# Kernel tuning notes

Hardware: AMD Instinct MI355X
Metric: run time of the kernel (lower is better)

## Reference

```python
import jax, jax.numpy as jnp
import numpy as np

NUM_TRACKS = [128, 256, 512, 1024, 2048, 64, 32, 1024]
B, S, D = 8, 2048, 1536
H = len(NUM_TRACKS)
T = max(NUM_TRACKS)  # num_output_tracks (padded)


def setup_inputs() -> dict:
    key = jax.random.key(0)
    kx, kw, kb, ki = jax.random.split(key, 4)
    x = jax.random.normal(kx, (B, S, D), dtype=jnp.float32)
    # Padded per-species weights: columns >= num_tracks[i] are zero, matching the
    # original's jnp.pad of head logits with zeros.
    track_mask = (jnp.arange(T)[None, :] < jnp.asarray(NUM_TRACKS)[:, None]).astype(jnp.float32)  # [H, T]
    W = jax.random.normal(kw, (H, D, T), dtype=jnp.float32) * 0.02
    W = W * track_mask[:, None, :]
    b = jax.random.normal(kb, (H, T), dtype=jnp.float32) * 0.02
    b = b * track_mask
    head_idx = jax.random.randint(ki, (B,), 0, H, dtype=jnp.int32)
    return {"x": x, "head_idx": head_idx, "W": W, "b": b}


def reference(x, head_idx, W, b):
    # Dense compute of ALL species heads (faithful to original which evaluates
    # every head over the full batch), then per-sample selection via head_idx
    # (equivalent to the original's sequential jnp.where masking).
    logits_all = jnp.einsum('bsd,hdt->bhst', x, W) + b[None, :, None, :]  # [B, H, S, T]
    sel = head_idx[:, None, None, None].astype(jnp.int32)                 # [B, 1, 1, 1]
    logits = jnp.take_along_axis(logits_all, sel, axis=1)[:, 0]           # [B, S, T]
    return logits
```

## Files before the change

### kernel.cpp

```cpp
#include <hip/hip_runtime.h>
#include <hip/hip_bf16.h>
#include <stdint.h>

#define NB 8
#define NS 2048
#define ND 1536
#define NT 2048
#define NH 8
#define NK2 (ND / 64)

__constant__ int c_tiles[NH] = {1, 2, 4, 8, 16, 1, 1, 8};

typedef short bf16x8 __attribute__((ext_vector_type(8)));
typedef unsigned short u16x8 __attribute__((ext_vector_type(8)));
typedef float f32x4 __attribute__((ext_vector_type(4)));

__device__ __forceinline__ unsigned short f2bf(float f) {
    union { float f; unsigned u; } a; a.f = f;
    unsigned r = a.u + 0x7fffu + ((a.u >> 16) & 1u);
    return (unsigned short)(r >> 16);
}

#define XBLK 24576
__global__ void cvt_kernel(const float* __restrict__ x,
                           const float* __restrict__ W,
                           const int* __restrict__ hidx,
                           unsigned short* __restrict__ xb,
                           unsigned short* __restrict__ Wt) {
    const int bid = blockIdx.x;
    const int tid = threadIdx.x;
    if (bid < XBLK) {
        const size_t i = (size_t)bid * 256 + tid;
        float4 v = ((const float4*)x)[i];
        ushort4 o;
        o.x = f2bf(v.x); o.y = f2bf(v.y); o.z = f2bf(v.z); o.w = f2bf(v.w);
        ((ushort4*)xb)[i] = o;
        return;
    }
    const int wid = bid - XBLK;
    const int h = wid / (32 * 24);
    const int rem = wid % (32 * 24);
    const int t0 = (rem % 32) * 64;
    const int d0 = (rem / 32) * 64;
    bool used = false;
    for (int i = 0; i < NB; ++i) used |= (hidx[i] == h);
    if (!used || t0 >= c_tiles[h] * 128) return;

    __shared__ float tile[64][69];
#pragma unroll
    for (int i = 0; i < 4; ++i) {
        const int idx = tid + i * 256;
        const int d = idx >> 4, c = (idx & 15) * 4;
        float4 v = *(const float4*)&W[((size_t)h * ND + d0 + d) * NT + t0 + c];
        tile[d][c] = v.x; tile[d][c + 1] = v.y;
        tile[d][c + 2] = v.z; tile[d][c + 3] = v.w;
    }
    __syncthreads();
    const int t = tid >> 2, dc = (tid & 3) * 16;
    u16x8 o0, o1;
#pragma unroll
    for (int j = 0; j < 8; ++j) o0[j] = f2bf(tile[dc + j][t]);
#pragma unroll
    for (int j = 0; j < 8; ++j) o1[j] = f2bf(tile[dc + 8 + j][t]);
    unsigned short* p = Wt + ((size_t)h * NT + t0 + t) * ND + d0 + dc;
    *(u16x8*)p = o0;
    *(u16x8*)(p + 8) = o1;
}

#define GLDS(g, l)                                                      \
    __builtin_amdgcn_global_load_lds(                                   \
        (const __attribute__((address_space(1))) void*)(g),             \
        (__attribute__((address_space(3))) void*)(l), 16, 0, 0)

__global__ __launch_bounds__(256) void gemm_kernel(
    const unsigned short* __restrict__ xb,
    const unsigned short* __restrict__ wt,
    const float* __restrict__ bias,
    const int* __restrict__ hidx,
    float* __restrict__ out)
{
    const int tid = threadIdx.x;
    const int id = blockIdx.x;

    int hh[NB], tl[NB];
    int P = 0;
#pragma unroll
    for (int b = 0; b < NB; ++b) {
        hh[b] = hidx[b];
        tl[b] = c_tiles[hh[b]];
        P += tl[b];
    }
    const int C = 16 * P;

    int batch, m0, n0;
    if (id >= C) {
        const int Pz = 128 - P;
        const int z = id - C;
        int p = z % Pz;
        const int m = z / Pz;
        int b = 0;
        while (p >= 16 - tl[b]) { p -= 16 - tl[b]; ++b; }
        batch = b; n0 = (tl[b] + p) * 128; m0 = m * 128;
        float* outb = out + (size_t)batch * NS * NT;
        const int row = tid >> 1;
        const int c0 = (tid & 1) * 64;
        float4 zv = make_float4(0.f, 0.f, 0.f, 0.f);
        float4* ptr = (float4*)(outb + (size_t)(m0 + row) * NT + (n0 + c0));
#pragma unroll
        for (int j = 0; j < 16; ++j) ptr[j] = zv;
        return;
    }
    {
        int p = id % P;
        const int m = id / P;
        int b = 0;
        while (p >= tl[b]) { p -= tl[b]; ++b; }
        batch = b; n0 = p * 128; m0 = m * 128;
    }
    const int h = hh[batch];
    float* outb = out + (size_t)batch * NS * NT;

    __shared__ unsigned short As[128 * 64];
    __shared__ unsigned short Bs[128 * 64];

    const int lane = tid & 63;
    const int wave = tid >> 6;
    const int wm = (wave >> 1) * 64;
    const int wn = (wave & 1) * 64;
    const int fr = lane & 15;
    const int q = lane >> 4;

    const unsigned short* ga[4];
    unsigned short* la[4];
#pragma unroll
    for (int j = 0; j < 4; ++j) {
        const int c = tid + 256 * j;
        const int r = c >> 3, gc = (c & 7) ^ (r & 7);
        ga[j] = xb + ((size_t)batch * NS + m0 + r) * ND + gc * 8;
        la[j] = As + c * 8;
    }
    const unsigned short* gb[4];
    unsigned short* lb[4];
#pragma unroll
    for (int j = 0; j < 4; ++j) {
        const int c = tid + 256 * j;
        const int r = c >> 3, gc = (c & 7) ^ (r & 7);
        gb[j] = wt + ((size_t)h * NT + n0 + r) * ND + gc * 8;
        lb[j] = Bs + c * 8;
    }

    const int sw0 = ((q) ^ (fr & 7)) * 8;
    const int sw1 = ((q + 4) ^ (fr & 7)) * 8;

    f32x4 acc[4][4] = {};

    for (int it = 0; it < NK2; ++it) {
#pragma unroll
        for (int j = 0; j < 4; ++j) GLDS(ga[j], la[j]);
#pragma unroll
        for (int j = 0; j < 4; ++j) GLDS(gb[j], lb[j]);
        __syncthreads();
#pragma unroll
        for (int kk = 0; kk < 2; ++kk) {
            const int sw = kk ? sw1 : sw0;
            bf16x8 af[4], bfr[4];
#pragma unroll
            for (int mi = 0; mi < 4; ++mi)
                af[mi] = *(const bf16x8*)(As + (wm + mi * 16 + fr) * 64 + sw);
#pragma unroll
            for (int ni = 0; ni < 4; ++ni)
                bfr[ni] = *(const bf16x8*)(Bs + (wn + ni * 16 + fr) * 64 + sw);
#pragma unroll
            for (int mi = 0; mi < 4; ++mi)
#pragma unroll
                for (int ni = 0; ni < 4; ++ni)
                    acc[mi][ni] = __builtin_amdgcn_mfma_f32_16x16x32_bf16(
                        af[mi], bfr[ni], acc[mi][ni], 0, 0, 0);
        }
        __syncthreads();
#pragma unroll
        for (int j = 0; j < 4; ++j) ga[j] += 64;
#pragma unroll
        for (int j = 0; j < 4; ++j) gb[j] += 64;
    }

    float bv[4];
#pragma unroll
    for (int ni = 0; ni < 4; ++ni)
        bv[ni] = bias[(size_t)h * NT + n0 + wn + ni * 16 + fr];

    const int rbase = m0 + wm + q * 4;
#pragma unroll
    for (int mi = 0; mi < 4; ++mi) {
#pragma unroll
        for (int r = 0; r < 4; ++r) {
            float* op = outb + (size_t)(rbase + mi * 16 + r) * NT + n0 + wn + fr;
#pragma unroll
            for (int ni = 0; ni < 4; ++ni)
                op[ni * 16] = acc[mi][ni][r] + bv[ni];
        }
    }
}

extern "C" void kernel_launch(void* const* d_in, const int* in_sizes, int n_in,
                              void* d_out, int out_size, void* d_ws, size_t ws_size,
                              hipStream_t stream) {
    const float* x    = (const float*)d_in[0];
    const int*   hidx = (const int*)d_in[1];
    const float* W    = (const float*)d_in[2];
    const float* bias = (const float*)d_in[3];
    float* out = (float*)d_out;

    unsigned short* xb = (unsigned short*)d_ws;
    unsigned short* wt = xb + (size_t)NB * NS * ND;

    cvt_kernel<<<dim3(XBLK + 32 * 24 * NH), dim3(256), 0, stream>>>(
        x, W, hidx, xb, wt);
    gemm_kernel<<<dim3(2048), dim3(256), 0, stream>>>(xb, wt, bias, hidx, out);
}
```

Baseline: 326.8 us.

## Double-buffer LDS tiles in bf16 GEMM to overlap loads with MFMA

```diff
diff --git a/kernel.cpp b/kernel.cpp
--- a/kernel.cpp
+++ b/kernel.cpp
@@ -120,8 +120,8 @@
     const int h = hh[batch];
     float* outb = out + (size_t)batch * NS * NT;
 
-    __shared__ unsigned short As[128 * 64];
-    __shared__ unsigned short Bs[128 * 64];
+    __shared__ unsigned short As[2][128 * 64];
+    __shared__ unsigned short Bs[2][128 * 64];
 
     const int lane = tid & 63;
     const int wave = tid >> 6;
@@ -131,22 +131,16 @@
     const int q = lane >> 4;
 
     const unsigned short* ga[4];
-    unsigned short* la[4];
+    const unsigned short* gb[4];
+    int ca[4], cb[4];
 #pragma unroll
     for (int j = 0; j < 4; ++j) {
         const int c = tid + 256 * j;
         const int r = c >> 3, gc = (c & 7) ^ (r & 7);
         ga[j] = xb + ((size_t)batch * NS + m0 + r) * ND + gc * 8;
-        la[j] = As + c * 8;
-    }
-    const unsigned short* gb[4];
-    unsigned short* lb[4];
-#pragma unroll
-    for (int j = 0; j < 4; ++j) {
-        const int c = tid + 256 * j;
-        const int r = c >> 3, gc = (c & 7) ^ (r & 7);
+        ca[j] = c * 8;
         gb[j] = wt + ((size_t)h * NT + n0 + r) * ND + gc * 8;
-        lb[j] = Bs + c * 8;
+        cb[j] = c * 8;
     }
 
     const int sw0 = ((q) ^ (fr & 7)) * 8;
@@ -154,35 +148,55 @@
 
     f32x4 acc[4][4] = {};
 
-    for (int it = 0; it < NK2; ++it) {
-#pragma unroll
-        for (int j = 0; j < 4; ++j) GLDS(ga[j], la[j]);
-#pragma unroll
-        for (int j = 0; j < 4; ++j) GLDS(gb[j], lb[j]);
+#define PREFETCH(B)                                                   \
+    do {                                                              \
+        _Pragma("unroll")                                             \
+        for (int j = 0; j < 4; ++j) GLDS(ga[j], &As[B][ca[j]]);       \
+        _Pragma("unroll")                                             \
+        for (int j = 0; j < 4; ++j) GLDS(gb[j], &Bs[B][cb[j]]);       \
+        _Pragma("unroll")                                             \
+        for (int j = 0; j < 4; ++j) { ga[j] += 64; gb[j] += 64; }     \
+    } while (0)
+
+#define COMPUTE(B)                                                            \
+    do {                                                                      \
+        _Pragma("unroll")                                                     \
+        for (int kk = 0; kk < 2; ++kk) {                                      \
+            const int sw = kk ? sw1 : sw0;                                    \
+            bf16x8 af[4], bfr[4];                                             \
+            _Pragma("unroll")                                                 \
+            for (int mi = 0; mi < 4; ++mi)                                    \
+                af[mi] = *(const bf16x8*)(&As[B][(wm + mi * 16 + fr) * 64 + sw]); \
+            _Pragma("unroll")                                                 \
+            for (int ni = 0; ni < 4; ++ni)                                    \
+                bfr[ni] = *(const bf16x8*)(&Bs[B][(wn + ni * 16 + fr) * 64 + sw]); \
+            _Pragma("unroll")                                                 \
+            for (int mi = 0; mi < 4; ++mi)                                    \
+                _Pragma("unroll")                                             \
+                for (int ni = 0; ni < 4; ++ni)                                \
+                    acc[mi][ni] = __builtin_amdgcn_mfma_f32_16x16x32_bf16(    \
+                        af[mi], bfr[ni], acc[mi][ni], 0, 0, 0);               \
+        }                                                                     \
+    } while (0)
+
+    PREFETCH(0);
+    __syncthreads();
+
+    for (int it = 0; it < 11; ++it) {
+        PREFETCH(1);
+        COMPUTE(0);
         __syncthreads();
-#pragma unroll
-        for (int kk = 0; kk < 2; ++kk) {
-            const int sw = kk ? sw1 : sw0;
-            bf16x8 af[4], bfr[4];
-#pragma unroll
-            for (int mi = 0; mi < 4; ++mi)
-                af[mi] = *(const bf16x8*)(As + (wm + mi * 16 + fr) * 64 + sw);
-#pragma unroll
-            for (int ni = 0; ni < 4; ++ni)
-                bfr[ni] = *(const bf16x8*)(Bs + (wn + ni * 16 + fr) * 64 + sw);
-#pragma unroll
-            for (int mi = 0; mi < 4; ++mi)
-#pragma unroll
-                for (int ni = 0; ni < 4; ++ni)
-                    acc[mi][ni] = __builtin_amdgcn_mfma_f32_16x16x32_bf16(
-                        af[mi], bfr[ni], acc[mi][ni], 0, 0, 0);
-        }
+        PREFETCH(0);
+        COMPUTE(1);
         __syncthreads();
-#pragma unroll
-        for (int j = 0; j < 4; ++j) ga[j] += 64;
-#pragma unroll
-        for (int j = 0; j < 4; ++j) gb[j] += 64;
-    }
+    }
+    PREFETCH(1);
+    COMPUTE(0);
+    __syncthreads();
+    COMPUTE(1);
+
+#undef PREFETCH
+#undef COMPUTE
 
     float bv[4];
 #pragma unroll
```

After: 335.8 us. +2.8%, slower.
